# Performance work log

Measured on AMD Instinct MI355X. Metric: run time of the kernel, lower is better.

The kernel has to match this reference:

```python
import jax, jax.numpy as jnp
import numpy as np

EPS = 1e-3  # keras BatchNormalization default epsilon


def _conv1x1(x, W, b):
    # x: (b, h, w, cin), W: (cin, cout)
    return jnp.einsum('bhwc,cd->bhwd', x, W) + b


def _bn(x, gamma, beta, mean, var):
    # inference-mode batch norm (moving statistics)
    return gamma * (x - mean) * jax.lax.rsqrt(var + EPS) + beta


def setup_inputs() -> dict:
    key = jax.random.key(0)
    ks = jax.random.split(key, 20)
    C, Ci = 512, 256
    B, Ha, Wa, Hd, Wd = 8, 32, 32, 64, 64
    s_in = 1.0 / np.sqrt(C)
    s_ic = 1.0 / np.sqrt(Ci)
    inp = {
        'detect': jax.random.normal(ks[0], (B, Hd, Wd, C), jnp.float32),
        'aim': jax.random.normal(ks[1], (B, Ha, Wa, C), jnp.float32),
        # g, theta, phi: C -> Ci 1x1 convs
        'Wg': jax.random.normal(ks[2], (C, Ci), jnp.float32) * s_in,
        'bg': jnp.zeros((Ci,), jnp.float32),
        'Wt': jax.random.normal(ks[3], (C, Ci), jnp.float32) * s_in,
        'bt': jnp.zeros((Ci,), jnp.float32),
        'Wp': jax.random.normal(ks[4], (C, Ci), jnp.float32) * s_in,
        'bp': jnp.zeros((Ci,), jnp.float32),
        # W branch: Ci -> C conv + BN
        'Ww': jax.random.normal(ks[5], (Ci, C), jnp.float32) * s_ic,
        'bw': jnp.zeros((C,), jnp.float32),
        'gw': jnp.ones((C,), jnp.float32),
        'betw': jnp.zeros((C,), jnp.float32),
        'mw': jax.random.normal(ks[6], (C,), jnp.float32) * 0.1,
        'vw': jax.random.uniform(ks[7], (C,), jnp.float32, 0.5, 1.5),
        # Q branch: Ci -> C conv + BN
        'Wq': jax.random.normal(ks[8], (Ci, C), jnp.float32) * s_ic,
        'bq': jnp.zeros((C,), jnp.float32),
        'gq': jnp.ones((C,), jnp.float32),
        'betq': jnp.zeros((C,), jnp.float32),
        'mq': jax.random.normal(ks[9], (C,), jnp.float32) * 0.1,
        'vq': jax.random.uniform(ks[10], (C,), jnp.float32, 0.5, 1.5),
    }
    return inp


def reference(detect, aim, Wg, bg, Wt, bt, Wp, bp,
              Ww, bw, gw, betw, mw, vw,
              Wq, bq, gq, betq, mq, vq):
    B, Ha, Wa, C = aim.shape
    _, Hd, Wd, _ = detect.shape
    Ci = Wg.shape[1]
    Na, Nd = Ha * Wa, Hd * Wd

    d_x = _conv1x1(detect, Wg, bg).reshape(B, Nd, Ci)     # (b, Nd, Ci)
    a_x = _conv1x1(aim, Wg, bg).reshape(B, Na, Ci)        # (b, Na, Ci)
    theta_x = _conv1x1(aim, Wt, bt).reshape(B, Na, Ci)    # (b, Na, Ci)
    phi_x = _conv1x1(detect, Wp, bp).reshape(B, Nd, Ci)   # (b, Nd, Ci)

    # affinity: (b, Na, Nd)
    f = jnp.einsum('bnc,bmc->bnm', theta_x, phi_x)
    f_div_C = f / Nd          # normalize by last dim of f
    fi_div_C = jnp.swapaxes(f, 1, 2) / Na  # (b, Nd, Na), normalized by its last dim

    non_aim = jnp.einsum('bnm,bmc->bnc', f_div_C, d_x).reshape(B, Ha, Wa, Ci)
    non_aim = _bn(_conv1x1(non_aim, Ww, bw), gw, betw, mw, vw) + aim

    non_det = jnp.einsum('bmn,bnc->bmc', fi_div_C, a_x).reshape(B, Hd, Wd, Ci)
    non_det = _bn(_conv1x1(non_det, Wq, bq), gq, betq, mq, vq) + detect

    return non_aim, non_det
```

## Files before the change

### kernel.cpp

```cpp
#include <hip/hip_runtime.h>

typedef unsigned short ushort_t;
typedef unsigned int uint32;
typedef __bf16 bf16x8 __attribute__((ext_vector_type(8)));
typedef float f32x4 __attribute__((ext_vector_type(4)));
typedef uint32 u32x4 __attribute__((ext_vector_type(4)));
typedef uint32 u32x2 __attribute__((ext_vector_type(2)));

typedef __attribute__((address_space(3))) uint32 as3_u32;
typedef const __attribute__((address_space(1))) uint32 as1_u32c;

__device__ __forceinline__ void gl_lds16(const ushort_t* g, ushort_t* l) {
    __builtin_amdgcn_global_load_lds((as1_u32c*)g, (as3_u32*)l, 16, 0, 0);
}

__device__ __forceinline__ float bf2f(ushort_t u) {
    uint32 x = ((uint32)u) << 16;
    return __builtin_bit_cast(float, x);
}
__device__ __forceinline__ ushort_t f2bf(float f) {
    uint32 x = __builtin_bit_cast(uint32, f);
    x += 0x7fffu + ((x >> 16) & 1u);
    return (ushort_t)(x >> 16);
}
__device__ __forceinline__ void ld4bf(const ushort_t* p, float* f) {
    const u32x2 w = *(const u32x2*)p;
    f[0] = bf2f((ushort_t)(w[0] & 0xffffu)); f[1] = bf2f((ushort_t)(w[0] >> 16));
    f[2] = bf2f((ushort_t)(w[1] & 0xffffu)); f[3] = bf2f((ushort_t)(w[1] >> 16));
}
__device__ __forceinline__ u32x2 pk4bf(const float* v) {
    u32x2 pk;
    pk[0] = (uint32)f2bf(v[0]) | ((uint32)f2bf(v[1]) << 16);
    pk[1] = (uint32)f2bf(v[2]) | ((uint32)f2bf(v[3]) << 16);
    return pk;
}

__device__ __forceinline__ bool sniff(const void* in0) {
    const uint32* s = (const uint32*)in0;
    const int lane = threadIdx.x & 63;
    int wd = 0;
    for (int c = 0; c < 4; c++) {
        const uint32 w = s[lane * 4 + c];
        const uint32 e = (w >> 7) & 0xFFu;
        wd += (e < 64u) || (e >= 192u);
    }
    for (int off = 32; off; off >>= 1) wd += __shfl_down(wd, off);
    return __shfl(wd, 0) > 32;
}

struct VecArgs { const void* s[14]; ushort_t* d[14]; int n[14]; };
struct WtArgs { const void* s[6]; ushort_t* d[6]; int R[6]; int C[6]; };
__global__ void canon_all(const void* __restrict__ dsrc, ushort_t* __restrict__ ddst,
                          const void* __restrict__ asrc, ushort_t* __restrict__ adst,
                          WtArgs wa, VecArgs va, int* __restrict__ flag) {
    const bool isf32 = sniff(dsrc);
    const int b = blockIdx.x;
    if (b < 3072) {
        const void* src; ushort_t* dst; long n; int b0, nb;
        if (b < 2048) { src = dsrc; dst = ddst; n = 16777216; b0 = b; nb = 2048; }
        else          { src = asrc; dst = adst; n = 4194304;  b0 = b - 2048; nb = 1024; }
        long i = ((long)b0 * 256 + threadIdx.x) * 8;
        const long stride = (long)nb * 256 * 8;
        if (isf32) {
            const float* s = (const float*)src;
            for (; i < n; i += stride) {
                const f32x4 a = *(const f32x4*)(s + i);
                const f32x4 c = *(const f32x4*)(s + i + 4);
                u32x4 o;
                o[0] = (uint32)f2bf(a[0]) | ((uint32)f2bf(a[1]) << 16);
                o[1] = (uint32)f2bf(a[2]) | ((uint32)f2bf(a[3]) << 16);
                o[2] = (uint32)f2bf(c[0]) | ((uint32)f2bf(c[1]) << 16);
                o[3] = (uint32)f2bf(c[2]) | ((uint32)f2bf(c[3]) << 16);
                *(u32x4*)(dst + i) = o;
            }
        } else {
            const ushort_t* s = (const ushort_t*)src;
            for (; i < n; i += stride)
                *(u32x4*)(dst + i) = *(const u32x4*)(s + i);
        }
    } else if (b < 4608) {
        const int local = b - 3072;
        const int wsel = local >> 8;
        const int rem = local & 255;
        const int tr = rem >> 4, tc = rem & 15;
        const int R = wa.R[wsel], C = wa.C[wsel];
        if (tc * 32 >= C || tr * 32 >= R) return;
        __shared__ float s[32][33];
        const int t = threadIdx.x;
        const int r = t >> 3, c4 = (t & 7) * 4;
        const long sbase = (long)(tr * 32 + r) * C + tc * 32 + c4;
        if (isf32) {
            const float* S = (const float*)wa.s[wsel];
            const f32x4 v = *(const f32x4*)(S + sbase);
            for (int u = 0; u < 4; u++) s[r][c4 + u] = v[u];
        } else {
            const ushort_t* S = (const ushort_t*)wa.s[wsel];
            for (int u = 0; u < 4; u++) s[r][c4 + u] = bf2f(S[sbase + u]);
        }
        __syncthreads();
        float tv[4];
        for (int u = 0; u < 4; u++) tv[u] = s[c4 + u][r];
        *(u32x2*)(wa.d[wsel] + (long)(tc * 32 + r) * R + tr * 32 + c4) = pk4bf(tv);
    } else {
        if (threadIdx.x == 0) *flag = isf32 ? 1 : 0;
        const int t = threadIdx.x;
        for (int seg = 0; seg < 14; seg++) {
            const int n = va.n[seg];
            if (isf32) {
                const float* s = (const float*)va.s[seg];
                for (int i = t; i < n; i += 256) va.d[seg][i] = f2bf(s[i]);
            } else {
                const ushort_t* s = (const ushort_t*)va.s[seg];
                for (int i = t; i < n; i += 256) va.d[seg][i] = s[i];
            }
        }
    }
}

__global__ void reduce_g_kernel(const float* __restrict__ P1, const float* __restrict__ P2,
                                ushort_t* __restrict__ G1, ushort_t* __restrict__ G2) {
    const int bxv = blockIdx.x;
    const int zz = bxv >> 6;
    const float* P = (zz < 8) ? P1 : P2;
    ushort_t* G    = (zz < 8) ? G1 : G2;
    const float alpha = (zz < 8) ? (1.f / 4096.f) : (1.f / 1024.f);
    const int b = zz & 7;
    const long off = ((long)(bxv & 63) * 256 + threadIdx.x) * 4;
    const float* base = P + (long)b * 8 * 65536 + off;
    f32x4 acc = {0.f, 0.f, 0.f, 0.f};
    for (int kc = 0; kc < 8; kc++) acc += *(const f32x4*)(base + (long)kc * 65536);
    float v[4] = {acc[0] * alpha, acc[1] * alpha, acc[2] * alpha, acc[3] * alpha};
    *(u32x2*)(G + (long)b * 65536 + off) = pk4bf(v);
}

#define BM 128
#define BN 128
#define BK 32
#define LDSH (BM * BK)
#define NBUF 3
#define BIGN (1 << 30)

enum { EPI_BIAS = 0, EPI_BIASR = 1, EPI_SCALE = 2, EPI_BN = 3, EPI_PART = 4 };

struct GP {
    const ushort_t* A; const ushort_t* B; void* Cv; ushort_t* CT;
    const ushort_t* bias; const ushort_t* gamma; const ushort_t* beta;
    const ushort_t* mean; const ushort_t* var; const ushort_t* res;
    long coff, sA, sB, sC;
    int K, lda, ldb, ldc, cnmax, ldT, bshift;
    float alpha;
};
struct GP2 { GP g[2]; };

template <int EPI, bool DYNOUT, bool DUALT, bool SWAP>
__global__ __launch_bounds__(256) void gemm_nt(GP2 ga, int ysplit, int zsplit,
                                               const int* __restrict__ flag)
{
    __shared__ __align__(16) ushort_t As[NBUF * LDSH];
    __shared__ __align__(16) ushort_t Bs[NBUF * LDSH];

    const bool isf32 = DYNOUT ? (*flag != 0) : false;

    const uint32 gx = gridDim.x, gy = gridDim.y;
    const uint32 nwg = gx * gy * gridDim.z;
    const uint32 lid = blockIdx.x + gx * (blockIdx.y + gy * blockIdx.z);
    const uint32 swz = (lid & 7u) * (nwg >> 3) + (lid >> 3);
    const uint32 bx = swz % gx, t1 = swz / gx;
    int by = (int)(t1 % gy), bz = (int)(t1 / gy);

    int sel = 0;
    if (by >= ysplit) { by -= ysplit; sel = 1; }
    if (bz >= zsplit) { bz -= zsplit; sel = 1; }
    const GP& p = ga.g[sel];

    const ushort_t* A = p.A + (long)bz * p.sA;
    const ushort_t* B = p.B + ((long)bz + (long)(by >> p.bshift)) * p.sB;
    const long cbase = p.coff + (long)bz * p.sC;
    const int lda = p.lda, ldb = p.ldb, ldc = p.ldc, K = p.K;

    const int tid  = threadIdx.x;
    const int lane = tid & 63;
    const int w    = tid >> 6;
    const int wr   = w >> 1, wc = w & 1;
    const int lr   = lane & 15, q = lane >> 4;

    const int m0 = by * BM;
    const int n0 = bx * BN;

    const int lrow = lane >> 2, lu = lane & 3;
    const int us = (lu ^ ((lrow >> 1) & 3)) * 8;
    const int ra0 = w * 32 + lrow, ra1 = w * 32 + 16 + lrow;
    const ushort_t* Ar0 = A + (long)(m0 + ra0) * lda + us;
    const ushort_t* Ar1 = A + (long)(m0 + ra1) * lda + us;
    const ushort_t* Br0 = B + (long)(n0 + ra0) * ldb + us;
    const ushort_t* Br1 = B + (long)(n0 + ra1) * ldb + us;
    ushort_t* sA0 = &As[(w * 2 + 0) * 512];
    ushort_t* sA1 = &As[(w * 2 + 1) * 512];
    ushort_t* sB0 = &Bs[(w * 2 + 0) * 512];
    ushort_t* sB1 = &Bs[(w * 2 + 1) * 512];

    const int swq = (q ^ ((lr >> 1) & 3)) * 8;

    f32x4 acc[4][4];
#pragma unroll
    for (int i = 0; i < 4; i++)
#pragma unroll
        for (int j = 0; j < 4; j++) acc[i][j] = (f32x4){0.f, 0.f, 0.f, 0.f};

    const int nt = K / BK;
    {
        gl_lds16(Ar0, sA0); gl_lds16(Ar1, sA1);
        gl_lds16(Br0, sB0); gl_lds16(Br1, sB1);
        if (nt > 1) {
            gl_lds16(Ar0 + BK, sA0 + LDSH); gl_lds16(Ar1 + BK, sA1 + LDSH);
            gl_lds16(Br0 + BK, sB0 + LDSH); gl_lds16(Br1 + BK, sB1 + LDSH);
        }
    }

    int c0 = 0, c2 = 2;
    for (int t = 0; t < nt; ++t) {
        if (t + 1 < nt) asm volatile("s_waitcnt vmcnt(4)" ::: "memory");
        else            asm volatile("s_waitcnt vmcnt(0)" ::: "memory");
        __builtin_amdgcn_s_barrier();
        __builtin_amdgcn_sched_barrier(0);

        if (t + 2 < nt) {
            const int nb = c2 * LDSH;
            const int kn = (t + 2) * BK;
            gl_lds16(Ar0 + kn, sA0 + nb); gl_lds16(Ar1 + kn, sA1 + nb);
            gl_lds16(Br0 + kn, sB0 + nb); gl_lds16(Br1 + kn, sB1 + nb);
        }
        __builtin_amdgcn_sched_barrier(0);

        const ushort_t* Ab = As + c0 * LDSH;
        const ushort_t* Bb = Bs + c0 * LDSH;
        bf16x8 af[4], bfr[4];
#pragma unroll
        for (int i = 0; i < 4; i++)
            af[i] = __builtin_bit_cast(bf16x8,
                *(const u32x4*)(&Ab[(wr * 64 + i * 16 + lr) * BK + swq]));
#pragma unroll
        for (int j = 0; j < 4; j++)
            bfr[j] = __builtin_bit_cast(bf16x8,
                *(const u32x4*)(&Bb[(wc * 64 + j * 16 + lr) * BK + swq]));
#pragma unroll
        for (int i = 0; i < 4; i++)
#pragma unroll
            for (int j = 0; j < 4; j++) {
                if constexpr (SWAP)
                    acc[i][j] = __builtin_amdgcn_mfma_f32_16x16x32_bf16(bfr[j], af[i], acc[i][j], 0, 0, 0);
                else
                    acc[i][j] = __builtin_amdgcn_mfma_f32_16x16x32_bf16(af[i], bfr[j], acc[i][j], 0, 0, 0);
            }
        __builtin_amdgcn_sched_barrier(0);

        c0 = (c0 + 1 == NBUF) ? 0 : c0 + 1;
        c2 = (c2 + 1 == NBUF) ? 0 : c2 + 1;
    }

    if constexpr (SWAP) {
#pragma unroll
        for (int j = 0; j < 4; j++) {
            const int coln = n0 + wc * 64 + j * 16 + q * 4;
            float sc4[4], sh4[4];
            if constexpr (EPI == EPI_BIAS) {
                float bb[4]; ld4bf(p.bias + coln, bb);
#pragma unroll
                for (int r = 0; r < 4; r++) { sc4[r] = 1.f; sh4[r] = bb[r]; }
            } else if constexpr (EPI == EPI_SCALE) {
#pragma unroll
                for (int r = 0; r < 4; r++) { sc4[r] = p.alpha; sh4[r] = 0.f; }
            } else if constexpr (EPI == EPI_BN) {
                float bb[4], g[4], bt[4], mn[4], vr[4];
                ld4bf(p.bias + coln, bb); ld4bf(p.gamma + coln, g); ld4bf(p.beta + coln, bt);
                ld4bf(p.mean + coln, mn); ld4bf(p.var + coln, vr);
#pragma unroll
                for (int r = 0; r < 4; r++) {
                    const float s = g[r] * rsqrtf(vr[r] + 1e-3f);
                    sc4[r] = s;
                    sh4[r] = s * bb[r] + bt[r] - s * mn[r];
                }
            }
#pragma unroll
            for (int i = 0; i < 4; i++) {
                const int row = m0 + wr * 64 + i * 16 + lr;
                const long off = cbase + (long)row * ldc + coln;
                float v[4];
#pragma unroll
                for (int r = 0; r < 4; r++) v[r] = acc[i][j][r];
                if constexpr (EPI == EPI_BIASR) {
                    const float bs = bf2f(p.bias[row]);
#pragma unroll
                    for (int r = 0; r < 4; r++) v[r] += bs;
                } else if constexpr (EPI == EPI_BN) {
                    float rs[4]; ld4bf(p.res + (long)row * ldc + coln, rs);
#pragma unroll
                    for (int r = 0; r < 4; r++) v[r] = sc4[r] * v[r] + sh4[r] + rs[r];
                } else if constexpr (EPI != EPI_PART) {
#pragma unroll
                    for (int r = 0; r < 4; r++) v[r] = sc4[r] * v[r] + sh4[r];
                }
                if constexpr (EPI == EPI_PART) {
                    *(f32x4*)((float*)p.Cv + off) = (f32x4){v[0], v[1], v[2], v[3]};
                } else if constexpr (DYNOUT) {
                    if (isf32) *(f32x4*)((float*)p.Cv + off) = (f32x4){v[0], v[1], v[2], v[3]};
                    else       *(u32x2*)((ushort_t*)p.Cv + off) = pk4bf(v);
                } else {
                    *(u32x2*)((ushort_t*)p.Cv + off) = pk4bf(v);
                }
            }
        }
    } else {
        const bool doC = (n0 < p.cnmax);
#pragma unroll
        for (int j = 0; j < 4; j++) {
            const int col = n0 + wc * 64 + j * 16 + lr;
            float bs = 0.f;
            if constexpr (EPI == EPI_BIAS) bs = bf2f(p.bias[col]);
#pragma unroll
            for (int i = 0; i < 4; i++) {
                const int rowbase = m0 + wr * 64 + i * 16 + q * 4;
                ushort_t tmp[4];
#pragma unroll
                for (int r = 0; r < 4; r++) {
                    const int row = rowbase + r;
                    float v = acc[i][j][r];
                    if constexpr (EPI == EPI_BIAS) v += bs;
                    else if constexpr (EPI == EPI_BIASR) v += bf2f(p.bias[row]);
                    else if constexpr (EPI == EPI_SCALE) v *= p.alpha;
                    const long off = cbase + (long)row * ldc + col;
                    if constexpr (EPI == EPI_PART) {
                        ((float*)p.Cv)[off] = v;
                    } else {
                        const ushort_t us2 = f2bf(v);
                        tmp[r] = us2;
                        if (doC) ((ushort_t*)p.Cv)[off] = us2;
                    }
                }
                if constexpr (DUALT) {
                    u32x2 pk;
                    pk[0] = (uint32)tmp[0] | ((uint32)tmp[1] << 16);
                    pk[1] = (uint32)tmp[2] | ((uint32)tmp[3] << 16);
                    *(u32x2*)(p.CT + (long)bz * p.sC + (long)col * p.ldT + rowbase) = pk;
                }
            }
        }
    }
}

extern "C" void kernel_launch(void* const* d_in, const int* in_sizes, int n_in,
                              void* d_out, int out_size, void* d_ws, size_t ws_size,
                              hipStream_t stream)
{
    int* flag = (int*)d_ws;
    ushort_t* base = (ushort_t*)((char*)d_ws + 16);
    long o = 0;
    ushort_t* detect_c = base + o; o += 16777216;
    ushort_t* aim_c    = base + o; o += 4194304;
    ushort_t* WpgT = base + o; o += 262144;
    ushort_t* WtgT = base + o; o += 262144;
    ushort_t* WwT  = base + o; o += 131072;
    ushort_t* WqT  = base + o; o += 131072;
    ushort_t* bpg_c  = base + o; o += 512;
    ushort_t* btg_c  = base + o; o += 512;
    ushort_t* bw_c   = base + o; o += 512;
    ushort_t* gw_c   = base + o; o += 512;
    ushort_t* betw_c = base + o; o += 512;
    ushort_t* mw_c   = base + o; o += 512;
    ushort_t* vw_c   = base + o; o += 512;
    ushort_t* bq_c   = base + o; o += 512;
    ushort_t* gq_c   = base + o; o += 512;
    ushort_t* betq_c = base + o; o += 512;
    ushort_t* mq_c   = base + o; o += 512;
    ushort_t* vq_c   = base + o; o += 512;
    ushort_t* phi    = base + o; o += 8388608;
    ushort_t* PT     = base + o; o += 16777216;
    ushort_t* theta  = base + o; o += 2097152;
    ushort_t* TT     = base + o; o += 4194304;
    ushort_t* G1     = base + o; o += 524288;
    ushort_t* G2     = base + o; o += 524288;
    ushort_t* M1T    = base + o; o += 1048576;
    ushort_t* M2T    = base + o; o += 1048576;
    ushort_t* U      = base + o; o += 16777216;
    float* P1 = (float*)U;
    float* P2 = P1 + 4194304;
    ushort_t* phiT = PT;
    ushort_t* d_xT = PT + 8388608;
    ushort_t* thetaT = TT;
    ushort_t* a_xT = TT + 2097152;

    VecArgs va;
    const int vidx[14] = {7, 3, 5, 3, 9, 10, 11, 12, 13, 15, 16, 17, 18, 19};
    ushort_t* vdst[14] = {bpg_c, bpg_c + 256, btg_c, btg_c + 256,
                          bw_c, gw_c, betw_c, mw_c, vw_c,
                          bq_c, gq_c, betq_c, mq_c, vq_c};
    const int vn[14] = {256, 256, 256, 256, 512, 512, 512, 512, 512, 512, 512, 512, 512, 512};
    for (int i = 0; i < 14; i++) { va.s[i] = d_in[vidx[i]]; va.d[i] = vdst[i]; va.n[i] = vn[i]; }

    WtArgs wa;
    wa.s[0] = d_in[6];  wa.d[0] = WpgT;              wa.R[0] = 512; wa.C[0] = 256;
    wa.s[1] = d_in[2];  wa.d[1] = WpgT + 256 * 512;  wa.R[1] = 512; wa.C[1] = 256;
    wa.s[2] = d_in[4];  wa.d[2] = WtgT;              wa.R[2] = 512; wa.C[2] = 256;
    wa.s[3] = d_in[2];  wa.d[3] = WtgT + 256 * 512;  wa.R[3] = 512; wa.C[3] = 256;
    wa.s[4] = d_in[8];  wa.d[4] = WwT;               wa.R[4] = 256; wa.C[4] = 512;
    wa.s[5] = d_in[14]; wa.d[5] = WqT;               wa.R[5] = 256; wa.C[5] = 512;

    canon_all<<<4609, 256, 0, stream>>>(d_in[0], detect_c, d_in[1], aim_c, wa, va, flag);

    const dim3 blk(256);
    const ushort_t* np = nullptr;
    ushort_t* npm = nullptr;

    {
        GP2 g;
        g.g[0] = GP{detect_c, WpgT, phi, PT, bpg_c, np, np, np, np, np,
                    0, 0, 0, 0, 512, 512, 512, 256, 256, 32768, 30, 1.f};
        g.g[1] = GP{aim_c, WtgT, theta, TT, btg_c, np, np, np, np, np,
                    0, 0, 0, 0, 512, 512, 512, 256, 256, 8192, 30, 1.f};
        gemm_nt<EPI_BIAS, false, true, false><<<dim3(4, 320, 1), blk, 0, stream>>>(
            g, 256, BIGN, flag);
    }

    {
        GP2 g;
        g.g[0] = GP{phiT, d_xT, P1, npm, np, np, np, np, np, np,
                    0, 512, 512, 65536, 512, 32768, 32768, 256, BIGN, 0, 30, 1.f};
        g.g[1] = GP{thetaT, a_xT, P2, npm, np, np, np, np, np, np,
                    0, 128, 128, 65536, 128, 8192, 8192, 256, BIGN, 0, 30, 1.f};
        gemm_nt<EPI_PART, false, false, true><<<dim3(2, 2, 128), blk, 0, stream>>>(
            g, BIGN, 64, flag);
    }

    reduce_g_kernel<<<1024, blk, 0, stream>>>(P1, P2, G1, G2);

    {
        GP2 g;
        g.g[0] = GP{G1, WwT, npm, M1T, np, np, np, np, np, np,
                    0, 65536, 0, 131072, 256, 256, 256, 512, 0, 256, 30, 1.f};
        g.g[1] = GP{G2, WqT, npm, M2T, np, np, np, np, np, np,
                    0, 65536, 0, 131072, 256, 256, 256, 512, 0, 256, 30, 1.f};
        gemm_nt<EPI_SCALE, false, true, false><<<dim3(4, 2, 16), blk, 0, stream>>>(
            g, BIGN, 8, flag);
    }

    {
        GP2 g;
        g.g[0] = GP{phi, M2T, d_out, npm, bq_c, gq_c, betq_c, mq_c, vq_c, detect_c,
                    8192L * 512, 0, 131072, 0, 256, 256, 256, 512, BIGN, 0, 5, 1.f};
        g.g[1] = GP{theta, M1T, d_out, npm, bw_c, gw_c, betw_c, mw_c, vw_c, aim_c,
                    0, 0, 131072, 0, 256, 256, 256, 512, BIGN, 0, 3, 1.f};
        gemm_nt<EPI_BN, true, false, true><<<dim3(4, 320, 1), blk, 0, stream>>>(
            g, 256, BIGN, flag);
    }
}
```

Measured before the change: 346.0 us.

## Fuse split-K partial reduction into GEMM via last-block atomic counter

Removes the separate reduce_g_kernel launch. The split-K partial GEMM now bumps a per-tile atomic counter, and the last of the eight contributing blocks sums the fp32 partials, scales them and writes the bf16 G tile. The canon conversion loop also handles 16 elements per thread and rebalances block counts between detect and aim. This adds a memset, fences and serialized tail work in the last block of each tile.

```diff
diff --git a/kernel.cpp b/kernel.cpp
--- a/kernel.cpp
+++ b/kernel.cpp
@@ -57,26 +57,37 @@
     const int b = blockIdx.x;
     if (b < 3072) {
         const void* src; ushort_t* dst; long n; int b0, nb;
-        if (b < 2048) { src = dsrc; dst = ddst; n = 16777216; b0 = b; nb = 2048; }
-        else          { src = asrc; dst = adst; n = 4194304;  b0 = b - 2048; nb = 1024; }
-        long i = ((long)b0 * 256 + threadIdx.x) * 8;
-        const long stride = (long)nb * 256 * 8;
+        if (b < 2560) { src = dsrc; dst = ddst; n = 16777216; b0 = b; nb = 2560; }
+        else          { src = asrc; dst = adst; n = 4194304;  b0 = b - 2560; nb = 512; }
+        long i = ((long)b0 * 256 + threadIdx.x) * 16;
+        const long stride = (long)nb * 256 * 16;
         if (isf32) {
             const float* s = (const float*)src;
             for (; i < n; i += stride) {
-                const f32x4 a = *(const f32x4*)(s + i);
-                const f32x4 c = *(const f32x4*)(s + i + 4);
-                u32x4 o;
-                o[0] = (uint32)f2bf(a[0]) | ((uint32)f2bf(a[1]) << 16);
-                o[1] = (uint32)f2bf(a[2]) | ((uint32)f2bf(a[3]) << 16);
-                o[2] = (uint32)f2bf(c[0]) | ((uint32)f2bf(c[1]) << 16);
-                o[3] = (uint32)f2bf(c[2]) | ((uint32)f2bf(c[3]) << 16);
-                *(u32x4*)(dst + i) = o;
+                const f32x4 a0 = *(const f32x4*)(s + i);
+                const f32x4 a1 = *(const f32x4*)(s + i + 4);
+                const f32x4 a2 = *(const f32x4*)(s + i + 8);
+                const f32x4 a3 = *(const f32x4*)(s + i + 12);
+                u32x4 o0, o1;
+                o0[0] = (uint32)f2bf(a0[0]) | ((uint32)f2bf(a0[1]) << 16);
+                o0[1] = (uint32)f2bf(a0[2]) | ((uint32)f2bf(a0[3]) << 16);
+                o0[2] = (uint32)f2bf(a1[0]) | ((uint32)f2bf(a1[1]) << 16);
+                o0[3] = (uint32)f2bf(a1[2]) | ((uint32)f2bf(a1[3]) << 16);
+                o1[0] = (uint32)f2bf(a2[0]) | ((uint32)f2bf(a2[1]) << 16);
+                o1[1] = (uint32)f2bf(a2[2]) | ((uint32)f2bf(a2[3]) << 16);
+                o1[2] = (uint32)f2bf(a3[0]) | ((uint32)f2bf(a3[1]) << 16);
+                o1[3] = (uint32)f2bf(a3[2]) | ((uint32)f2bf(a3[3]) << 16);
+                *(u32x4*)(dst + i) = o0;
+                *(u32x4*)(dst + i + 8) = o1;
             }
         } else {
             const ushort_t* s = (const ushort_t*)src;
-            for (; i < n; i += stride)
-                *(u32x4*)(dst + i) = *(const u32x4*)(s + i);
+            for (; i < n; i += stride) {
+                const u32x4 v0 = *(const u32x4*)(s + i);
+                const u32x4 v1 = *(const u32x4*)(s + i + 8);
+                *(u32x4*)(dst + i) = v0;
+                *(u32x4*)(dst + i + 8) = v1;
+            }
         }
     } else if (b < 4608) {
         const int local = b - 3072;
@@ -117,22 +128,6 @@
     }
 }
 
-__global__ void reduce_g_kernel(const float* __restrict__ P1, const float* __restrict__ P2,
-                                ushort_t* __restrict__ G1, ushort_t* __restrict__ G2) {
-    const int bxv = blockIdx.x;
-    const int zz = bxv >> 6;
-    const float* P = (zz < 8) ? P1 : P2;
-    ushort_t* G    = (zz < 8) ? G1 : G2;
-    const float alpha = (zz < 8) ? (1.f / 4096.f) : (1.f / 1024.f);
-    const int b = zz & 7;
-    const long off = ((long)(bxv & 63) * 256 + threadIdx.x) * 4;
-    const float* base = P + (long)b * 8 * 65536 + off;
-    f32x4 acc = {0.f, 0.f, 0.f, 0.f};
-    for (int kc = 0; kc < 8; kc++) acc += *(const f32x4*)(base + (long)kc * 65536);
-    float v[4] = {acc[0] * alpha, acc[1] * alpha, acc[2] * alpha, acc[3] * alpha};
-    *(u32x2*)(G + (long)b * 65536 + off) = pk4bf(v);
-}
-
 #define BM 128
 #define BN 128
 #define BK 32
@@ -149,6 +144,7 @@
     long coff, sA, sB, sC;
     int K, lda, ldb, ldc, cnmax, ldT, bshift;
     float alpha;
+    uint32* cnt;
 };
 struct GP2 { GP g[2]; };
 
@@ -346,6 +342,37 @@
             }
         }
     }
+
+    if constexpr (EPI == EPI_PART) {
+        __shared__ int lastf;
+        __syncthreads();
+        if (tid == 0) {
+            __threadfence();
+            const int cidx = sel * 32 + (int)(bz >> 3) * 4 + by * 2 + (int)bx;
+            lastf = (atomicAdd(p.cnt + cidx, 1u) == 7u) ? 1 : 0;
+        }
+        __syncthreads();
+        if (lastf) {
+            if (tid == 0) __threadfence();
+            __syncthreads();
+            const int bq = (int)(bz >> 3);
+            const float* Pb = (const float*)p.Cv + (long)bq * 8 * 65536;
+            ushort_t* Gout = p.CT + (long)bq * 65536;
+            const long qoff = (long)(by * 128) * 256 + (long)bx * 128;
+            for (int t2 = tid; t2 < 4096; t2 += 256) {
+                const int rr = t2 >> 5;
+                const int cc = (t2 & 31) * 4;
+                const long po = qoff + (long)rr * 256 + cc;
+                f32x4 s4 = {0.f, 0.f, 0.f, 0.f};
+#pragma unroll
+                for (int kc = 0; kc < 8; kc++)
+                    s4 += *(const f32x4*)(Pb + (long)kc * 65536 + po);
+                float v[4] = {s4[0] * p.alpha, s4[1] * p.alpha,
+                              s4[2] * p.alpha, s4[3] * p.alpha};
+                *(u32x2*)(Gout + po) = pk4bf(v);
+            }
+        }
+    }
 }
 
 extern "C" void kernel_launch(void* const* d_in, const int* in_sizes, int n_in,
@@ -353,7 +380,8 @@
                               hipStream_t stream)
 {
     int* flag = (int*)d_ws;
-    ushort_t* base = (ushort_t*)((char*)d_ws + 16);
+    uint32* cnt = (uint32*)((char*)d_ws + 64);
+    ushort_t* base = (ushort_t*)((char*)d_ws + 512);
     long o = 0;
     ushort_t* detect_c = base + o; o += 16777216;
     ushort_t* aim_c    = base + o; o += 4194304;
@@ -389,6 +417,8 @@
     ushort_t* thetaT = TT;
     ushort_t* a_xT = TT + 2097152;
 
+    hipMemsetAsync(cnt, 0, 256, stream);
+
     VecArgs va;
     const int vidx[14] = {7, 3, 5, 3, 9, 10, 11, 12, 13, 15, 16, 17, 18, 19};
     ushort_t* vdst[14] = {bpg_c, bpg_c + 256, btg_c, btg_c + 256,
@@ -423,15 +453,15 @@
 
     {
         GP2 g;
-        g.g[0] = GP{phiT, d_xT, P1, npm, np, np, np, np, np, np,
-                    0, 512, 512, 65536, 512, 32768, 32768, 256, BIGN, 0, 30, 1.f};
-        g.g[1] = GP{thetaT, a_xT, P2, npm, np, np, np, np, np, np,
-                    0, 128, 128, 65536, 128, 8192, 8192, 256, BIGN, 0, 30, 1.f};
+        g.g[0] = GP{phiT, d_xT, P1, G1, np, np, np, np, np, np,
+                    0, 512, 512, 65536, 512, 32768, 32768, 256, BIGN, 0, 30, 1.f / 4096.f};
+        g.g[1] = GP{thetaT, a_xT, P2, G2, np, np, np, np, np, np,
+                    0, 128, 128, 65536, 128, 8192, 8192, 256, BIGN, 0, 30, 1.f / 1024.f};
+        g.g[0].cnt = cnt;
+        g.g[1].cnt = cnt;
         gemm_nt<EPI_PART, false, false, true><<<dim3(2, 2, 128), blk, 0, stream>>>(
             g, BIGN, 64, flag);
     }
-
-    reduce_g_kernel<<<1024, blk, 0, stream>>>(P1, P2, G1, G2);
 
     {
         GP2 g;
```

Result: no change. 347.8 us (+0.5%).
